# Kernel optimization log

Hardware: AMD Instinct MI355X
Metric: run time of the kernel (lower is better)

The kernel has to match this reference:

```python
import jax, jax.numpy as jnp
import numpy as np

N = 65536      # number of points
D = 3          # spatial dimension (init arg 'dimension')
C = 64         # feature channels
K = 16         # neighbors returned by faiss knn search
BLOCK = 512    # query block size for chunked brute-force distances
GRID = 128     # spatial_size


def setup_inputs() -> dict:
    key = jax.random.key(0)
    k1, k2 = jax.random.split(key)
    coords = jax.random.randint(k1, (N, D), 0, GRID, dtype=jnp.int32)
    features = jax.random.normal(k2, (N, C), dtype=jnp.float32)
    return {"coords": coords, "features": features}


def reference(coords, features):
    """Brute-force KNN over integer point coords (faiss-equivalent exact L2
    search), then sparse input-layer construction: for each point, gather the
    features of its K nearest neighbors and sum them (SCN InputLayer mode=3)."""
    cf = coords.astype(jnp.float32)                 # [N, D]
    db_sq = jnp.sum(cf * cf, axis=1)                # [N]

    n_blocks = N // BLOCK
    queries = cf.reshape(n_blocks, BLOCK, D)

    def step(_, q):                                 # q: [BLOCK, D]
        q_sq = jnp.sum(q * q, axis=1)               # [BLOCK]
        # squared L2 distances to all database points: [BLOCK, N]
        dist = q_sq[:, None] - 2.0 * (q @ cf.T) + db_sq[None, :]
        _, idx = jax.lax.top_k(-dist, K)            # [BLOCK, K] nearest indices
        nb = features[idx]                          # irregular gather [BLOCK, K, C]
        return None, jnp.sum(nb, axis=1)            # mode=3: sum duplicates/neighbors

    _, out = jax.lax.scan(step, None, queries)      # [n_blocks, BLOCK, C]
    return out.reshape(N, C)
```

## Files before the change

### kernel.cpp

```cpp
#include <hip/hip_runtime.h>


typedef unsigned int uint;
typedef unsigned short ushort;
typedef short short2v __attribute__((ext_vector_type(2)));
typedef uint u32x4 __attribute__((ext_vector_type(4), aligned(8)));

#define NPTS   65536
#define NCELL  32768

static __device__ inline short2v u2s(uint v) { union { uint u; short2v s; } c; c.u = v; return c.s; }
static __device__ inline uint s2u(short2v v) { union { uint u; short2v s; } c; c.s = v; return c.u; }

static __device__ inline int dot2acc(short2v a, short2v b, int c) {
#if __has_builtin(__builtin_amdgcn_sdot2)
    return __builtin_amdgcn_sdot2(a, b, c, false);
#else
    return (int)a.x * (int)b.x + (int)a.y * (int)b.y + c;
#endif
}

__global__ __launch_bounds__(256) void cell_count(const int* __restrict__ coords,
                                                  uint* __restrict__ counts) {
    int i = blockIdx.x * 256 + threadIdx.x;
    int x = coords[3 * i + 0], y = coords[3 * i + 1], z = coords[3 * i + 2];
    int cell = (x >> 2) | ((y >> 2) << 5) | ((z >> 2) << 10);
    atomicAdd(&counts[cell], 1u);
}

__global__ __launch_bounds__(256) void chunk_reduce(const uint* __restrict__ counts,
                                                    uint* __restrict__ chunktot) {
    __shared__ uint wsum[4];
    int tid = threadIdx.x;
    int lane = tid & 63, wv = tid >> 6;
    uint c = counts[blockIdx.x * 256 + tid];
#pragma unroll
    for (int off = 32; off; off >>= 1) c += __shfl_xor(c, off, 64);
    if (lane == 0) wsum[wv] = c;
    __syncthreads();
    if (tid == 0) chunktot[blockIdx.x] = wsum[0] + wsum[1] + wsum[2] + wsum[3];
}

__global__ __launch_bounds__(256) void scan_chunk(const uint* __restrict__ counts,
                                                  const uint* __restrict__ chunktot,
                                                  uint* __restrict__ starts,
                                                  uint* __restrict__ cursors) {
    __shared__ uint wsum[4];
    int b = blockIdx.x;
    int tid = threadIdx.x;
    int lane = tid & 63, wv = tid >> 6;
    int cell = b * 256 + tid;

    uint t0 = chunktot[lane];
    uint t1 = chunktot[64 + lane];
    uint s = (lane < b ? t0 : 0u) + (64 + lane < b ? t1 : 0u);
#pragma unroll
    for (int off = 32; off; off >>= 1) s += __shfl_xor(s, off, 64);
    uint base = s;

    uint c = counts[cell];
    uint v = c;
#pragma unroll
    for (int off = 1; off < 64; off <<= 1) {
        uint u = __shfl_up(v, off, 64);
        if (lane >= off) v += u;
    }
    if (lane == 63) wsum[wv] = v;
    __syncthreads();
    uint woff = 0;
#pragma unroll
    for (int j = 0; j < 4; ++j) woff += (j < wv) ? wsum[j] : 0u;
    uint st = base + woff + v - c;
    starts[cell]  = st;
    cursors[cell] = st;
    if (cell == NCELL - 1) starts[NCELL] = st + c;
}

__global__ __launch_bounds__(256) void cell_scatter(const int* __restrict__ coords,
                                                    uint* __restrict__ cursors,
                                                    uint2* __restrict__ sorted) {
    int i = blockIdx.x * 256 + threadIdx.x;
    int x = coords[3 * i + 0], y = coords[3 * i + 1], z = coords[3 * i + 2];
    int cell = (x >> 2) | ((y >> 2) << 5) | ((z >> 2) << 10);
    uint pos = atomicAdd(&cursors[cell], 1u);
    sorted[pos] = make_uint2((uint)(x | (y << 16)), (uint)(i | (z << 16)));
}

__global__ __launch_bounds__(256, 4) void knn_search(const uint* __restrict__ starts,
                                                     const uint2* __restrict__ sorted,
                                                     const float* __restrict__ feat,
                                                     float* __restrict__ out) {
    int blk  = (blockIdx.x & 7) * 128 + (blockIdx.x >> 3);
    int wave = threadIdx.x >> 6;
    int lane = threadIdx.x & 63;
    int qslot = lane & 15;
    int slice = lane >> 4;
    int qpos = blk * 64 + wave * 16 + qslot;

    uint2 me = sorted[qpos];
    uint qxy = me.x;
    uint qzp = me.y & 0xFFFF0000u;
    uint qidx = me.y & 0xFFFFu;
    int qx = (int)(me.x & 0xFFFFu);
    int qy = (int)(me.x >> 16);
    int qz = (int)(me.y >> 16);
    int cx = qx >> 2, cy = qy >> 2, cz = qz >> 2;

    uint k[16];
#pragma unroll
    for (int j = 0; j < 16; ++j) k[j] = 0xFFFFFFFFu;

    auto insert1 = [&](uint2 pt) {
        short2v A = u2s(pt.x) - u2s(qxy);
        short2v B = u2s(pt.y) - u2s(qzp);
        uint Bu = s2u(B);
        short2v Bm = u2s(Bu & 0xFFFF0000u);
        int d2 = dot2acc(A, A, dot2acc(Bm, Bm, 0));
        uint key = ((uint)d2 << 16) + (Bu & 0xFFFFu);
#pragma unroll
        for (int j = 15; j >= 1; --j)
            asm("v_med3_u32 %0, %1, %2, %3"
                : "=v"(k[j]) : "v"(k[j - 1]), "v"(k[j]), "v"(key));
        k[0] = min(k[0], key);
    };

    auto scan4 = [&](uint p0, uint p1) {
        for (uint p = p0 + (uint)slice; p < p1; p += 4u) insert1(sorted[p]);
    };

    auto merge_min = [&](int mask) {
        uint b[16];
#pragma unroll
        for (int j = 0; j < 16; ++j) b[j] = __shfl_xor(k[j], mask, 64);
#pragma unroll
        for (int j = 0; j < 16; ++j) k[j] = min(k[j], b[15 - j]);
    };
    auto clean = [&]() {
#pragma unroll
        for (int d = 8; d >= 1; d >>= 1) {
#pragma unroll
            for (int i = 0; i < 16; ++i) {
                if ((i & d) == 0) {
                    uint lo = min(k[i], k[i + d]);
                    uint hi = max(k[i], k[i + d]);
                    k[i] = lo;
                    k[i + d] = hi;
                }
            }
        }
    };
    auto merge = [&](int mask) { merge_min(mask); clean(); };
    auto merge_all = [&]() { merge(16); merge(32); };

    int xa = min(max(cx - ((qx & 3) < 2 ? 2 : 1), 0), 28);
    int ya = min(max(cy - ((qy & 3) < 2 ? 2 : 1), 0), 28);
    int za = min(max(cz - ((qz & 3) < 2 ? 2 : 1), 0), 28);

    {
        int ybase = (ya + slice) << 5;
        int rb0 = ybase | ((za + 0) << 10);
        int rb1 = ybase | ((za + 1) << 10);
        int rb2 = ybase | ((za + 2) << 10);
        int rb3 = ybase | ((za + 3) << 10);
        uint pA = starts[rb0 + xa], eA = starts[rb0 + xa + 4];
        uint pB = starts[rb1 + xa], eB = starts[rb1 + xa + 4];
        uint pC = starts[rb2 + xa], eC = starts[rb2 + xa + 4];
        uint pD = starts[rb3 + xa], eD = starts[rb3 + xa + 4];
        while (__any((pA < eA) || (pB < eB) || (pC < eC) || (pD < eD))) {
            bool a0 = pA < eA, a1 = pA + 1 < eA;
            bool b0 = pB < eB, b1 = pB + 1 < eB;
            bool c0 = pC < eC, c1 = pC + 1 < eC;
            bool d0 = pD < eD, d1 = pD + 1 < eD;
            u32x4 VA, VB, VC, VD;
            if (a0) VA = *reinterpret_cast<const u32x4*>(sorted + pA);
            if (b0) VB = *reinterpret_cast<const u32x4*>(sorted + pB);
            if (c0) VC = *reinterpret_cast<const u32x4*>(sorted + pC);
            if (d0) VD = *reinterpret_cast<const u32x4*>(sorted + pD);
            pA += (a0 ? 1u : 0u) + (a1 ? 1u : 0u);
            pB += (b0 ? 1u : 0u) + (b1 ? 1u : 0u);
            pC += (c0 ? 1u : 0u) + (c1 ? 1u : 0u);
            pD += (d0 ? 1u : 0u) + (d1 ? 1u : 0u);
            if (a0) insert1(make_uint2(VA.x, VA.y));
            if (b0) insert1(make_uint2(VB.x, VB.y));
            if (c0) insert1(make_uint2(VC.x, VC.y));
            if (d0) insert1(make_uint2(VD.x, VD.y));
            if (a1) insert1(make_uint2(VA.z, VA.w));
            if (b1) insert1(make_uint2(VB.z, VB.w));
            if (c1) insert1(make_uint2(VC.z, VC.w));
            if (d1) insert1(make_uint2(VD.z, VD.w));
        }
    }
    merge(16); merge_min(32);
    uint mx = k[0];
#pragma unroll
    for (int j = 1; j < 16; ++j) mx = max(mx, k[j]);

    bool redo = (mx >> 16) >= 49u;
    if (__any(redo)) {
        clean();
        if (redo || slice != 0) {
#pragma unroll
            for (int j = 0; j < 16; ++j) k[j] = 0xFFFFFFFFu;
        }
        if (redo) {
            int xl = max(cx - 2, 0), xh = min(cx + 2, 31);
            int yl = max(cy - 2, 0), yh = min(cy + 2, 31);
            int zl = max(cz - 2, 0), zh = min(cz + 2, 31);
            for (int z = zl; z <= zh; ++z)
                for (int y = yl; y <= yh; ++y) {
                    int rb = (y << 5) | (z << 10);
                    scan4(starts[rb + xl], starts[rb + xh + 1]);
                }
        }
        merge_all();
        for (int r = 3; r < 32; ++r) {
            uint b = (uint)(4 * r - 3);
            bool active = (k[15] >> 16) >= b * b;
            if (!__any(active)) break;
            if (slice != 0) {
#pragma unroll
                for (int j = 0; j < 16; ++j) k[j] = 0xFFFFFFFFu;
            }
            if (active) {
                int z0 = cz - r < 0 ? 0 : cz - r;
                int z1 = cz + r > 31 ? 31 : cz + r;
                for (int z = z0; z <= z1; ++z) {
                    bool zface = (z == cz - r) || (z == cz + r);
                    int y0 = cy - r < 0 ? 0 : cy - r;
                    int y1 = cy + r > 31 ? 31 : cy + r;
                    for (int y = y0; y <= y1; ++y) {
                        bool face = zface || (y == cy - r) || (y == cy + r);
                        int rb = (y << 5) | (z << 10);
                        if (face) {
                            int x0 = cx - r < 0 ? 0 : cx - r;
                            int x1 = cx + r > 31 ? 31 : cx + r;
                            scan4(starts[rb + x0], starts[rb + x1 + 1]);
                        } else {
                            int xL = cx - r;
                            if (xL >= 0) scan4(starts[rb + xL], starts[rb + xL + 1]);
                            int xR = cx + r;
                            if (xR <= 31) scan4(starts[rb + xR], starts[rb + xR + 1]);
                        }
                    }
                }
            }
            merge_all();
        }
    }

    uint ki[16];
#pragma unroll
    for (int j = 0; j < 16; ++j) ki[j] = k[j] & 0xFFFFu;

    int ch = lane & 15;
    int qg = lane >> 4;
#pragma unroll
    for (int p = 0; p < 4; ++p) {
        int qs = p * 4 + qg;
        uint qorig = __shfl(qidx, qs, 64);
        float4 acc = make_float4(0.f, 0.f, 0.f, 0.f);
#pragma unroll
        for (int j = 0; j < 16; ++j) {
            uint nj = __shfl(ki[j], qs, 64);
            float4 v = reinterpret_cast<const float4*>(feat)[nj * 16u + (uint)ch];
            acc.x += v.x; acc.y += v.y; acc.z += v.z; acc.w += v.w;
        }
        reinterpret_cast<float4*>(out)[qorig * 16u + (uint)ch] = acc;
    }
}

extern "C" void kernel_launch(void* const* d_in, const int* in_sizes, int n_in,
                              void* d_out, int out_size, void* d_ws, size_t ws_size,
                              hipStream_t stream) {
    const int*   coords = (const int*)d_in[0];
    const float* feat   = (const float*)d_in[1];
    float*       out    = (float*)d_out;

    uint* W = (uint*)d_ws;
    uint*  chunktot = W;
    uint*  counts   = W + 128;
    uint*  starts   = W + 32896;
    uint*  cursors  = W + 65668;
    uint2* sorted   = (uint2*)(W + 98436);

    hipMemsetAsync(counts, 0, NCELL * sizeof(uint), stream);
    cell_count<<<NPTS / 256, 256, 0, stream>>>(coords, counts);
    chunk_reduce<<<NCELL / 256, 256, 0, stream>>>(counts, chunktot);
    scan_chunk<<<NCELL / 256, 256, 0, stream>>>(counts, chunktot, starts, cursors);
    cell_scatter<<<NPTS / 256, 256, 0, stream>>>(coords, cursors, sorted);
    knn_search<<<1024, 256, 0, stream>>>(starts, sorted, feat, out);
}
```

Before: 61.59 us.

## Stage region candidate points in LDS and use one thread per query

Replaces the per-query wave search (4 lanes splitting cells and merging through shuffles) with a region-based kernel. Each block owns a 4x4x4 cell region, stages the surrounding 8x8x8 cell halo's points into shared memory, and lets each thread run a full 4x4x4-cell search for one query out of LDS. The aim is to reuse candidate loads across queries and remove the cross-lane merges. In exchange, per-thread work becomes serial and load-imbalanced, occupancy drops to 2 blocks per SM, grid size halves, and regions that overflow the caps fall back to global memory (queries past the 512 cap would be dropped).

Result: slower. 101.0 us (+64.0%).

```diff
diff --git a/kernel.cpp b/kernel.cpp
--- a/kernel.cpp
+++ b/kernel.cpp
@@ -4,10 +4,11 @@
 typedef unsigned int uint;
 typedef unsigned short ushort;
 typedef short short2v __attribute__((ext_vector_type(2)));
-typedef uint u32x4 __attribute__((ext_vector_type(4), aligned(8)));
-
-#define NPTS   65536
-#define NCELL  32768
+
+#define NPTS     65536
+#define NCELL    32768
+#define CAND_CAP 1664
+#define QCAP     512
 
 static __device__ inline short2v u2s(uint v) { union { uint u; short2v s; } c; c.u = v; return c.s; }
 static __device__ inline uint s2u(short2v v) { union { uint u; short2v s; } c; c.s = v; return c.u; }
@@ -86,186 +87,206 @@
     sorted[pos] = make_uint2((uint)(x | (y << 16)), (uint)(i | (z << 16)));
 }
 
-__global__ __launch_bounds__(256, 4) void knn_search(const uint* __restrict__ starts,
+__global__ __launch_bounds__(256, 2) void knn_region(const uint* __restrict__ starts,
                                                      const uint2* __restrict__ sorted,
                                                      const float* __restrict__ feat,
                                                      float* __restrict__ out) {
-    int blk  = (blockIdx.x & 7) * 128 + (blockIdx.x >> 3);
-    int wave = threadIdx.x >> 6;
-    int lane = threadIdx.x & 63;
-    int qslot = lane & 15;
-    int slice = lane >> 4;
-    int qpos = blk * 64 + wave * 16 + qslot;
-
-    uint2 me = sorted[qpos];
-    uint qxy = me.x;
-    uint qzp = me.y & 0xFFFF0000u;
-    uint qidx = me.y & 0xFFFFu;
-    int qx = (int)(me.x & 0xFFFFu);
-    int qy = (int)(me.x >> 16);
-    int qz = (int)(me.y >> 16);
-    int cx = qx >> 2, cy = qy >> 2, cz = qz >> 2;
-
-    uint k[16];
-#pragma unroll
-    for (int j = 0; j < 16; ++j) k[j] = 0xFFFFFFFFu;
-
-    auto insert1 = [&](uint2 pt) {
-        short2v A = u2s(pt.x) - u2s(qxy);
-        short2v B = u2s(pt.y) - u2s(qzp);
-        uint Bu = s2u(B);
-        short2v Bm = u2s(Bu & 0xFFFF0000u);
-        int d2 = dot2acc(A, A, dot2acc(Bm, Bm, 0));
-        uint key = ((uint)d2 << 16) + (Bu & 0xFFFFu);
-#pragma unroll
-        for (int j = 15; j >= 1; --j)
-            asm("v_med3_u32 %0, %1, %2, %3"
-                : "=v"(k[j]) : "v"(k[j - 1]), "v"(k[j]), "v"(key));
-        k[0] = min(k[0], key);
-    };
-
-    auto scan4 = [&](uint p0, uint p1) {
-        for (uint p = p0 + (uint)slice; p < p1; p += 4u) insert1(sorted[p]);
-    };
-
-    auto merge_min = [&](int mask) {
-        uint b[16];
-#pragma unroll
-        for (int j = 0; j < 16; ++j) b[j] = __shfl_xor(k[j], mask, 64);
-#pragma unroll
-        for (int j = 0; j < 16; ++j) k[j] = min(k[j], b[15 - j]);
-    };
-    auto clean = [&]() {
-#pragma unroll
-        for (int d = 8; d >= 1; d >>= 1) {
-#pragma unroll
-            for (int i = 0; i < 16; ++i) {
-                if ((i & d) == 0) {
-                    uint lo = min(k[i], k[i + d]);
-                    uint hi = max(k[i], k[i + d]);
-                    k[i] = lo;
-                    k[i + d] = hi;
-                }
+    __shared__ uint2  cand[CAND_CAP];
+    __shared__ uint   rowlo[65];
+    __shared__ uint   rowgs[64];
+    __shared__ ushort bnd[64][9];
+    __shared__ uint   qlist[QCAP];
+    __shared__ uint   gt[256 * 17];
+    __shared__ uint   nq_sh, stot_sh;
+
+    int b = (blockIdx.x & 7) * 64 + (blockIdx.x >> 3);
+    int Rx = (b & 7) * 4, Ry = ((b >> 3) & 7) * 4, Rz = (b >> 6) * 4;
+    int x0  = max(Rx - 2, 0); int nx = min(Rx + 6, 32) - x0;
+    int ys0 = max(Ry - 2, 0); int ny = min(Ry + 6, 32) - ys0;
+    int zs0 = max(Rz - 2, 0); int nz = min(Rz + 6, 32) - zs0;
+
+    int tid = threadIdx.x, lane = tid & 63, wv = tid >> 6;
+
+    if (wv == 0) {
+        int yi = lane & 7, zi = lane >> 3;
+        bool valid = (yi < ny) && (zi < nz);
+        uint gs = 0, len = 0;
+        if (valid) {
+            int rb = ((ys0 + yi) << 5) | ((zs0 + zi) << 10);
+            gs  = starts[rb + x0];
+            len = starts[rb + x0 + nx] - gs;
+        }
+        uint v = len;
+#pragma unroll
+        for (int off = 1; off < 64; off <<= 1) {
+            uint u = __shfl_up(v, off, 64);
+            if (lane >= off) v += u;
+        }
+        rowlo[lane] = v - len;
+        rowgs[lane] = gs;
+        if (lane == 63) { rowlo[64] = v; stot_sh = v; }
+    } else if (wv == 1 && lane < 16) {
+        int qy = lane & 3, qz = lane >> 2;
+        int rb = ((Ry + qy) << 5) | ((Rz + qz) << 10);
+        uint g0  = starts[rb + Rx];
+        uint len = starts[rb + Rx + 4] - g0;
+        uint v = len;
+#pragma unroll
+        for (int off = 1; off < 16; off <<= 1) {
+            uint u = __shfl_up(v, off, 64);
+            if (lane >= off) v += u;
+        }
+        uint e0 = v - len;
+        for (uint j = 0; j < len; ++j)
+            if (e0 + j < QCAP) qlist[e0 + j] = g0 + j;
+        if (lane == 15) nq_sh = min(v, (uint)QCAP);
+    }
+    __syncthreads();
+
+    uint stot = stot_sh;
+    bool ofl  = stot > CAND_CAP;
+    uint nq   = nq_sh;
+
+    for (int e = tid; e < 576; e += 256) {
+        int r = e / 9, i = e - r * 9;
+        int yi = r & 7, zi = r >> 3;
+        if (yi < ny && zi < nz && i <= nx) {
+            int rb = ((ys0 + yi) << 5) | ((zs0 + zi) << 10);
+            bnd[r][i] = (ushort)(rowlo[r] + (starts[rb + x0 + i] - rowgs[r]));
+        }
+    }
+    if (!ofl) {
+        for (int r = wv; r < 64; r += 4) {
+            uint lo = rowlo[r], len = rowlo[r + 1] - lo, gs = rowgs[r];
+            for (uint p = lane; p < len; p += 64) cand[lo + p] = sorted[gs + p];
+        }
+    }
+    __syncthreads();
+
+    for (uint cbase = 0; cbase < nq; cbase += 256) {
+        bool have = (cbase + (uint)tid) < nq;
+        uint k[16];
+#pragma unroll
+        for (int j = 0; j < 16; ++j) k[j] = 0xFFFFFFFFu;
+
+        uint qxy = 0, qzp = 0, qidx = 0;
+        int qx = 0, qy = 0, qz = 0, cx = 0, cy = 0, cz = 0;
+        if (have) {
+            uint2 me = sorted[qlist[cbase + tid]];
+            qxy = me.x; qzp = me.y & 0xFFFF0000u; qidx = me.y & 0xFFFFu;
+            qx = (int)(me.x & 0xFFFFu); qy = (int)(me.x >> 16); qz = (int)(me.y >> 16);
+            cx = qx >> 2; cy = qy >> 2; cz = qz >> 2;
+        }
+
+        auto insert1 = [&](uint2 pt) {
+            short2v A = u2s(pt.x) - u2s(qxy);
+            short2v B = u2s(pt.y) - u2s(qzp);
+            uint Bu = s2u(B);
+            short2v Bm = u2s(Bu & 0xFFFF0000u);
+            int d2 = dot2acc(A, A, dot2acc(Bm, Bm, 0));
+            uint key = ((uint)d2 << 16) + (Bu & 0xFFFFu);
+#pragma unroll
+            for (int j = 15; j >= 1; --j)
+                asm("v_med3_u32 %0, %1, %2, %3"
+                    : "=v"(k[j]) : "v"(k[j - 1]), "v"(k[j]), "v"(key));
+            k[0] = min(k[0], key);
+        };
+
+        int xa = min(max(cx - ((qx & 3) < 2 ? 2 : 1), 0), 28);
+        int ya = min(max(cy - ((qy & 3) < 2 ? 2 : 1), 0), 28);
+        int za = min(max(cz - ((qz & 3) < 2 ? 2 : 1), 0), 28);
+
+        if (have) {
+            if (!ofl) {
+                int i0 = xa - x0, ry0 = ya - ys0, rz0 = za - zs0;
+#pragma unroll
+                for (int rz = 0; rz < 4; ++rz)
+#pragma unroll
+                    for (int ry = 0; ry < 4; ++ry) {
+                        int r = (rz0 + rz) * 8 + (ry0 + ry);
+                        uint p0 = bnd[r][i0], p1 = bnd[r][i0 + 4];
+                        for (uint p = p0; p < p1; ++p) insert1(cand[p]);
+                    }
+            } else {
+                for (int rz = 0; rz < 4; ++rz)
+                    for (int ry = 0; ry < 4; ++ry) {
+                        int rb = ((ya + ry) << 5) | ((za + rz) << 10);
+                        uint p1 = starts[rb + xa + 4];
+                        for (uint p = starts[rb + xa]; p < p1; ++p) insert1(sorted[p]);
+                    }
             }
         }
-    };
-    auto merge = [&](int mask) { merge_min(mask); clean(); };
-    auto merge_all = [&]() { merge(16); merge(32); };
-
-    int xa = min(max(cx - ((qx & 3) < 2 ? 2 : 1), 0), 28);
-    int ya = min(max(cy - ((qy & 3) < 2 ? 2 : 1), 0), 28);
-    int za = min(max(cz - ((qz & 3) < 2 ? 2 : 1), 0), 28);
-
-    {
-        int ybase = (ya + slice) << 5;
-        int rb0 = ybase | ((za + 0) << 10);
-        int rb1 = ybase | ((za + 1) << 10);
-        int rb2 = ybase | ((za + 2) << 10);
-        int rb3 = ybase | ((za + 3) << 10);
-        uint pA = starts[rb0 + xa], eA = starts[rb0 + xa + 4];
-        uint pB = starts[rb1 + xa], eB = starts[rb1 + xa + 4];
-        uint pC = starts[rb2 + xa], eC = starts[rb2 + xa + 4];
-        uint pD = starts[rb3 + xa], eD = starts[rb3 + xa + 4];
-        while (__any((pA < eA) || (pB < eB) || (pC < eC) || (pD < eD))) {
-            bool a0 = pA < eA, a1 = pA + 1 < eA;
-            bool b0 = pB < eB, b1 = pB + 1 < eB;
-            bool c0 = pC < eC, c1 = pC + 1 < eC;
-            bool d0 = pD < eD, d1 = pD + 1 < eD;
-            u32x4 VA, VB, VC, VD;
-            if (a0) VA = *reinterpret_cast<const u32x4*>(sorted + pA);
-            if (b0) VB = *reinterpret_cast<const u32x4*>(sorted + pB);
-            if (c0) VC = *reinterpret_cast<const u32x4*>(sorted + pC);
-            if (d0) VD = *reinterpret_cast<const u32x4*>(sorted + pD);
-            pA += (a0 ? 1u : 0u) + (a1 ? 1u : 0u);
-            pB += (b0 ? 1u : 0u) + (b1 ? 1u : 0u);
-            pC += (c0 ? 1u : 0u) + (c1 ? 1u : 0u);
-            pD += (d0 ? 1u : 0u) + (d1 ? 1u : 0u);
-            if (a0) insert1(make_uint2(VA.x, VA.y));
-            if (b0) insert1(make_uint2(VB.x, VB.y));
-            if (c0) insert1(make_uint2(VC.x, VC.y));
-            if (d0) insert1(make_uint2(VD.x, VD.y));
-            if (a1) insert1(make_uint2(VA.z, VA.w));
-            if (b1) insert1(make_uint2(VB.z, VB.w));
-            if (c1) insert1(make_uint2(VC.z, VC.w));
-            if (d1) insert1(make_uint2(VD.z, VD.w));
-        }
-    }
-    merge(16); merge_min(32);
-    uint mx = k[0];
-#pragma unroll
-    for (int j = 1; j < 16; ++j) mx = max(mx, k[j]);
-
-    bool redo = (mx >> 16) >= 49u;
-    if (__any(redo)) {
-        clean();
-        if (redo || slice != 0) {
-#pragma unroll
-            for (int j = 0; j < 16; ++j) k[j] = 0xFFFFFFFFu;
-        }
-        if (redo) {
-            int xl = max(cx - 2, 0), xh = min(cx + 2, 31);
-            int yl = max(cy - 2, 0), yh = min(cy + 2, 31);
-            int zl = max(cz - 2, 0), zh = min(cz + 2, 31);
-            for (int z = zl; z <= zh; ++z)
-                for (int y = yl; y <= yh; ++y) {
-                    int rb = (y << 5) | (z << 10);
-                    scan4(starts[rb + xl], starts[rb + xh + 1]);
-                }
-        }
-        merge_all();
-        for (int r = 3; r < 32; ++r) {
-            uint b = (uint)(4 * r - 3);
-            bool active = (k[15] >> 16) >= b * b;
-            if (!__any(active)) break;
-            if (slice != 0) {
+
+        bool redo = have && ((k[15] >> 16) >= 49u);
+        if (__any(redo)) {
+            if (redo) {
 #pragma unroll
                 for (int j = 0; j < 16; ++j) k[j] = 0xFFFFFFFFu;
-            }
-            if (active) {
-                int z0 = cz - r < 0 ? 0 : cz - r;
-                int z1 = cz + r > 31 ? 31 : cz + r;
-                for (int z = z0; z <= z1; ++z) {
-                    bool zface = (z == cz - r) || (z == cz + r);
-                    int y0 = cy - r < 0 ? 0 : cy - r;
-                    int y1 = cy + r > 31 ? 31 : cy + r;
-                    for (int y = y0; y <= y1; ++y) {
-                        bool face = zface || (y == cy - r) || (y == cy + r);
+                int xl = max(cx - 2, 0), xh = min(cx + 2, 31);
+                int yl = max(cy - 2, 0), yh = min(cy + 2, 31);
+                int zl = max(cz - 2, 0), zh = min(cz + 2, 31);
+                for (int z = zl; z <= zh; ++z)
+                    for (int y = yl; y <= yh; ++y) {
                         int rb = (y << 5) | (z << 10);
-                        if (face) {
-                            int x0 = cx - r < 0 ? 0 : cx - r;
-                            int x1 = cx + r > 31 ? 31 : cx + r;
-                            scan4(starts[rb + x0], starts[rb + x1 + 1]);
-                        } else {
-                            int xL = cx - r;
-                            if (xL >= 0) scan4(starts[rb + xL], starts[rb + xL + 1]);
-                            int xR = cx + r;
-                            if (xR <= 31) scan4(starts[rb + xR], starts[rb + xR + 1]);
+                        uint p1 = starts[rb + xh + 1];
+                        for (uint p = starts[rb + xl]; p < p1; ++p) insert1(sorted[p]);
+                    }
+                for (int r = 3; r < 32; ++r) {
+                    uint bb = (uint)(4 * r - 3);
+                    if ((k[15] >> 16) < bb * bb) break;
+                    int z0 = max(cz - r, 0), z1 = min(cz + r, 31);
+                    for (int z = z0; z <= z1; ++z) {
+                        bool zface = (z == cz - r) || (z == cz + r);
+                        int y0 = max(cy - r, 0), y1 = min(cy + r, 31);
+                        for (int y = y0; y <= y1; ++y) {
+                            bool face = zface || (y == cy - r) || (y == cy + r);
+                            int rb = (y << 5) | (z << 10);
+                            if (face) {
+                                int xf0 = max(cx - r, 0), xf1 = min(cx + r, 31);
+                                uint p1 = starts[rb + xf1 + 1];
+                                for (uint p = starts[rb + xf0]; p < p1; ++p) insert1(sorted[p]);
+                            } else {
+                                int xL = cx - r;
+                                if (xL >= 0) {
+                                    uint p1 = starts[rb + xL + 1];
+                                    for (uint p = starts[rb + xL]; p < p1; ++p) insert1(sorted[p]);
+                                }
+                                int xR = cx + r;
+                                if (xR <= 31) {
+                                    uint p1 = starts[rb + xR + 1];
+                                    for (uint p = starts[rb + xR]; p < p1; ++p) insert1(sorted[p]);
+                                }
+                            }
                         }
                     }
                 }
             }
-            merge_all();
-        }
-    }
-
-    uint ki[16];
-#pragma unroll
-    for (int j = 0; j < 16; ++j) ki[j] = k[j] & 0xFFFFu;
-
-    int ch = lane & 15;
-    int qg = lane >> 4;
-#pragma unroll
-    for (int p = 0; p < 4; ++p) {
-        int qs = p * 4 + qg;
-        uint qorig = __shfl(qidx, qs, 64);
-        float4 acc = make_float4(0.f, 0.f, 0.f, 0.f);
-#pragma unroll
-        for (int j = 0; j < 16; ++j) {
-            uint nj = __shfl(ki[j], qs, 64);
-            float4 v = reinterpret_cast<const float4*>(feat)[nj * 16u + (uint)ch];
-            acc.x += v.x; acc.y += v.y; acc.z += v.z; acc.w += v.w;
-        }
-        reinterpret_cast<float4*>(out)[qorig * 16u + (uint)ch] = acc;
+        }
+
+        if (have) {
+            gt[tid * 17] = qidx;
+#pragma unroll
+            for (int j = 0; j < 16; ++j) gt[tid * 17 + 1 + j] = k[j] & 0xFFFFu;
+        }
+        __syncthreads();
+
+        uint cn = min(nq - cbase, 256u);
+        int ch = lane & 15, qg = lane >> 4;
+        for (uint ps = wv; ps * 4 < cn; ps += 4) {
+            uint qs = ps * 4 + (uint)qg;
+            if (qs < cn) {
+                uint qorig = gt[qs * 17];
+                float4 acc = make_float4(0.f, 0.f, 0.f, 0.f);
+#pragma unroll
+                for (int j = 0; j < 16; ++j) {
+                    uint nj = gt[qs * 17 + 1 + j];
+                    float4 v = reinterpret_cast<const float4*>(feat)[nj * 16u + (uint)ch];
+                    acc.x += v.x; acc.y += v.y; acc.z += v.z; acc.w += v.w;
+                }
+                reinterpret_cast<float4*>(out)[qorig * 16u + (uint)ch] = acc;
+            }
+        }
+        __syncthreads();
     }
 }
 
@@ -288,5 +309,5 @@
     chunk_reduce<<<NCELL / 256, 256, 0, stream>>>(counts, chunktot);
     scan_chunk<<<NCELL / 256, 256, 0, stream>>>(counts, chunktot, starts, cursors);
     cell_scatter<<<NPTS / 256, 256, 0, stream>>>(coords, cursors, sorted);
-    knn_search<<<1024, 256, 0, stream>>>(starts, sorted, feat, out);
-}
+    knn_region<<<512, 256, 0, stream>>>(starts, sorted, feat, out);
+}
```

## Fuse scan kernels, split feature gather into separate kernel, simplify merge

Applied to the files above, without the earlier changes.

Merges the chunk reduction and the scan into one kernel, where each block sums all preceding counts directly, removing one launch. The knn kernel now runs a full merge and writes 16-bit neighbor indices to a workspace buffer. A new gather kernel reads those indices and sums the features with coalesced per-query rows. This trades an extra launch and a round trip through global memory for a lighter knn kernel, and the redundant prefix reads in the scan grow with block index.

Result: slower. 225.0 us (+265.3%).

```diff
diff --git a/kernel.cpp b/kernel.cpp
--- a/kernel.cpp
+++ b/kernel.cpp
@@ -28,35 +28,22 @@
     atomicAdd(&counts[cell], 1u);
 }
 
-__global__ __launch_bounds__(256) void chunk_reduce(const uint* __restrict__ counts,
-                                                    uint* __restrict__ chunktot) {
-    __shared__ uint wsum[4];
-    int tid = threadIdx.x;
-    int lane = tid & 63, wv = tid >> 6;
-    uint c = counts[blockIdx.x * 256 + tid];
-#pragma unroll
-    for (int off = 32; off; off >>= 1) c += __shfl_xor(c, off, 64);
-    if (lane == 0) wsum[wv] = c;
-    __syncthreads();
-    if (tid == 0) chunktot[blockIdx.x] = wsum[0] + wsum[1] + wsum[2] + wsum[3];
-}
-
-__global__ __launch_bounds__(256) void scan_chunk(const uint* __restrict__ counts,
-                                                  const uint* __restrict__ chunktot,
+__global__ __launch_bounds__(256) void scan_fused(const uint* __restrict__ counts,
                                                   uint* __restrict__ starts,
                                                   uint* __restrict__ cursors) {
     __shared__ uint wsum[4];
+    __shared__ uint rsum[4];
     int b = blockIdx.x;
     int tid = threadIdx.x;
     int lane = tid & 63, wv = tid >> 6;
     int cell = b * 256 + tid;
 
-    uint t0 = chunktot[lane];
-    uint t1 = chunktot[64 + lane];
-    uint s = (lane < b ? t0 : 0u) + (64 + lane < b ? t1 : 0u);
-#pragma unroll
-    for (int off = 32; off; off >>= 1) s += __shfl_xor(s, off, 64);
-    uint base = s;
+    uint acc = 0;
+    int lim = b * 256;
+    for (int j = tid; j < lim; j += 256) acc += counts[j];
+#pragma unroll
+    for (int off = 32; off; off >>= 1) acc += __shfl_xor(acc, off, 64);
+    if (lane == 0) rsum[wv] = acc;
 
     uint c = counts[cell];
     uint v = c;
@@ -67,6 +54,7 @@
     }
     if (lane == 63) wsum[wv] = v;
     __syncthreads();
+    uint base = rsum[0] + rsum[1] + rsum[2] + rsum[3];
     uint woff = 0;
 #pragma unroll
     for (int j = 0; j < 4; ++j) woff += (j < wv) ? wsum[j] : 0u;
@@ -88,8 +76,7 @@
 
 __global__ __launch_bounds__(256, 4) void knn_search(const uint* __restrict__ starts,
                                                      const uint2* __restrict__ sorted,
-                                                     const float* __restrict__ feat,
-                                                     float* __restrict__ out) {
+                                                     uint2* __restrict__ nbr) {
     int blk  = (blockIdx.x & 7) * 128 + (blockIdx.x >> 3);
     int wave = threadIdx.x >> 6;
     int lane = threadIdx.x & 63;
@@ -190,14 +177,10 @@
             if (d1) insert1(make_uint2(VD.z, VD.w));
         }
     }
-    merge(16); merge_min(32);
-    uint mx = k[0];
-#pragma unroll
-    for (int j = 1; j < 16; ++j) mx = max(mx, k[j]);
-
-    bool redo = (mx >> 16) >= 49u;
+    merge_all();
+
+    bool redo = (k[15] >> 16) >= 49u;
     if (__any(redo)) {
-        clean();
         if (redo || slice != 0) {
 #pragma unroll
             for (int j = 0; j < 16; ++j) k[j] = 0xFFFFFFFFu;
@@ -248,25 +231,27 @@
         }
     }
 
-    uint ki[16];
-#pragma unroll
-    for (int j = 0; j < 16; ++j) ki[j] = k[j] & 0xFFFFu;
-
-    int ch = lane & 15;
-    int qg = lane >> 4;
-#pragma unroll
-    for (int p = 0; p < 4; ++p) {
-        int qs = p * 4 + qg;
-        uint qorig = __shfl(qidx, qs, 64);
-        float4 acc = make_float4(0.f, 0.f, 0.f, 0.f);
-#pragma unroll
-        for (int j = 0; j < 16; ++j) {
-            uint nj = __shfl(ki[j], qs, 64);
-            float4 v = reinterpret_cast<const float4*>(feat)[nj * 16u + (uint)ch];
-            acc.x += v.x; acc.y += v.y; acc.z += v.z; acc.w += v.w;
-        }
-        reinterpret_cast<float4*>(out)[qorig * 16u + (uint)ch] = acc;
-    }
+    int s4 = slice * 4;
+    uint w0 = (k[s4 + 0] & 0xFFFFu) | (k[s4 + 1] << 16);
+    uint w1 = (k[s4 + 2] & 0xFFFFu) | (k[s4 + 3] << 16);
+    nbr[qidx * 4u + (uint)slice] = make_uint2(w0, w1);
+}
+
+__global__ __launch_bounds__(256) void gather(const ushort* __restrict__ nbr,
+                                              const float* __restrict__ feat,
+                                              float* __restrict__ out) {
+    int g = blockIdx.x * 256 + threadIdx.x;
+    int q = g >> 4, ch = g & 15;
+    int lane = threadIdx.x & 63;
+    uint nv = nbr[q * 16 + ch];
+    float4 acc = make_float4(0.f, 0.f, 0.f, 0.f);
+#pragma unroll
+    for (int j = 0; j < 16; ++j) {
+        uint nj = __shfl(nv, (lane & 48) + j, 64);
+        float4 v = reinterpret_cast<const float4*>(feat)[nj * 16u + (uint)ch];
+        acc.x += v.x; acc.y += v.y; acc.z += v.z; acc.w += v.w;
+    }
+    reinterpret_cast<float4*>(out)[(uint)q * 16u + (uint)ch] = acc;
 }
 
 extern "C" void kernel_launch(void* const* d_in, const int* in_sizes, int n_in,
@@ -277,16 +262,16 @@
     float*       out    = (float*)d_out;
 
     uint* W = (uint*)d_ws;
-    uint*  chunktot = W;
-    uint*  counts   = W + 128;
-    uint*  starts   = W + 32896;
-    uint*  cursors  = W + 65668;
-    uint2* sorted   = (uint2*)(W + 98436);
+    uint*  counts  = W;
+    uint*  starts  = W + 32768;
+    uint*  cursors = W + 65540;
+    uint2* sorted  = (uint2*)(W + 98308);
+    uint2* nbr     = (uint2*)(W + 229384);
 
     hipMemsetAsync(counts, 0, NCELL * sizeof(uint), stream);
     cell_count<<<NPTS / 256, 256, 0, stream>>>(coords, counts);
-    chunk_reduce<<<NCELL / 256, 256, 0, stream>>>(counts, chunktot);
-    scan_chunk<<<NCELL / 256, 256, 0, stream>>>(counts, chunktot, starts, cursors);
+    scan_fused<<<NCELL / 256, 256, 0, stream>>>(counts, starts, cursors);
     cell_scatter<<<NPTS / 256, 256, 0, stream>>>(coords, cursors, sorted);
-    knn_search<<<1024, 256, 0, stream>>>(starts, sorted, feat, out);
-}
+    knn_search<<<1024, 256, 0, stream>>>(starts, sorted, nbr);
+    gather<<<NPTS * 16 / 256, 256, 0, stream>>>((const ushort*)nbr, feat, out);
+}
```
